# Optimization experiments

Hardware: AMD Instinct MI355X
Metric: run time of the kernel (lower is better)

Reference implementation:

```python
import jax, jax.numpy as jnp
from jax import lax
import numpy as np

# ---- config (repo globals, scaled to a 112x112 feature map of a 448 image) ----
IMG, FEAT = 448, 112
PSTRIDE = IMG // FEAT  # 4 pixels per feature cell
RATIOS = [(16, 16), (12, 20), (20, 12),
          (24, 24), (20, 28), (28, 20),
          (32, 32), (24, 40), (40, 24), (28, 40), (40, 28), (28, 36), (36, 28)]
GROUPS = [(0, 3), (3, 6), (6, 13)]   # ratio groups per NMS scale
N_LIST = [2, 3, 2]
IOU_THRESHS = [0.25, 0.25, 0.25]
BATCH = 256
WINDOW_NUMS = [(FEAT - rh + 1) * (FEAT - rw + 1) for rh, rw in RATIOS]
TOTAL = sum(WINDOW_NUMS)             # 96981
PROPOSALN = sum(N_LIST)              # 7


def _coordinates():
    # Mirrors ComputeCoordinate: box = [x0,y0,x1,y1] in pixels, lefttop clipped to 0.
    parts = []
    for rh, rw in RATIOS:
        nr, nc = FEAT - rh + 1, FEAT - rw + 1
        xi = np.repeat(np.arange(nr), nc).astype(np.float32)
        yi = np.tile(np.arange(nc), nr).astype(np.float32)
        x0 = xi * PSTRIDE - 1.0
        y0 = yi * PSTRIDE - 1.0
        x1 = x0 + rh * PSTRIDE
        y1 = y0 + rw * PSTRIDE
        x0 = np.maximum(x0, 0.0)
        y0 = np.maximum(y0, 0.0)
        parts.append(np.stack([x0, y0, x1, y1], 1))
    return np.concatenate(parts, 0).astype(np.float32)  # (TOTAL, 4)


def setup_inputs() -> dict:
    key = jax.random.key(0)
    x = jax.random.normal(key, (BATCH, 1, FEAT, FEAT), jnp.float32)
    coords = jnp.asarray(_coordinates())
    return {"x": x, "coords": coords, "proposalN": PROPOSALN}


def _nms(scores, coords, n_pick, thresh):
    # Greedy NMS: repeatedly take best-scoring alive window, suppress IoU > thresh.
    # If everything is suppressed before n_pick picks, repeat the last pick (repo behavior).
    areas = (coords[:, 2] - coords[:, 0] + 1.0) * (coords[:, 3] - coords[:, 1] + 1.0)

    def step(state, _):
        alive, last = state
        any_alive = jnp.any(alive)
        idx = jnp.where(any_alive,
                        jnp.argmax(jnp.where(alive, scores, -jnp.inf)).astype(jnp.int32),
                        last)
        box = coords[idx]
        lt = jnp.maximum(coords[:, :2], box[:2])
        rb = jnp.minimum(coords[:, 2:], box[2:])
        w = rb[:, 0] - lt[:, 0] + 1.0
        h = rb[:, 1] - lt[:, 1] + 1.0
        inter = jnp.where((w < 0) | (h < 0), 0.0, w * h)
        iou = inter / (areas + areas[idx] - inter)
        keep = (alive & (iou <= thresh)).at[idx].set(False)
        return (jnp.where(any_alive, keep, alive), idx), idx

    init = (jnp.ones(scores.shape[0], bool), jnp.int32(0))
    return lax.scan(step, init, None, length=n_pick)[1]  # (n_pick,) int32


def _forward(x, coords):
    B = x.shape[0]
    # multiscale sliding-window average scores (AvgPool2d, stride 1, VALID)
    avgs = [lax.reduce_window(x, 0.0, lax.add, (1, 1, rh, rw), (1, 1, 1, 1), 'VALID')
            .reshape(B, -1) / float(rh * rw) for rh, rw in RATIOS]
    all_scores = jnp.concatenate(avgs, 1)  # (B, TOTAL)

    idx_parts = []
    for j, (g0, g1) in enumerate(GROUPS):
        s0 = int(sum(WINDOW_NUMS[:g0]))
        s1 = int(sum(WINDOW_NUMS[:g1]))
        cd = coords[s0:s1]
        nms_j = lambda s, cd=cd, j=j: _nms(s, cd, N_LIST[j], IOU_THRESHS[j])
        picks = jax.vmap(nms_j)(all_scores[:, s0:s1])  # (B, N_LIST[j])
        idx_parts.append(picks + s0)
    proposalN_indices = jnp.concatenate(idx_parts, 1)  # (B, PROPOSALN)
    proposalN_windows_scores = jnp.take_along_axis(all_scores, proposalN_indices, 1)
    window_scores = all_scores  # reshape(batch, -1) of all_scores
    return proposalN_indices, proposalN_windows_scores, window_scores


def reference(x, coords, proposalN):
    assert proposalN == PROPOSALN
    return _forward(x, coords)
```

## Files before the change

kernel.cpp:

```cpp
#include <hip/hip_runtime.h>
#include <math.h>
#include <limits.h>

namespace {
constexpr int kFeat = 112;
constexpr int kBatch = 256;
constexpr int kTotal = 96981;
constexpr int kStride = 115;
constexpr int kNT = 1024;
constexpr int kRH[13] = {16,12,20,24,20,28,32,24,40,28,40,28,36};
constexpr int kRW[13] = {16,20,12,24,28,20,32,40,24,40,28,36,28};
constexpr int kOff[13] = {0,9409,18802,28195,36116,44021,51926,58487,64984,71481,77686,83891,90436};
}

struct NmsShared {
  float rs[kNT / 64];
  int   ri[kNT / 64];
  float shS; int shI;
  float pX0[3], pY0[3], pX1[3], pY1[3], pA[3];
  int   pI[3];
};

__device__ inline void block_argmax(float s, int i, NmsShared* ns) {
  __syncthreads();
#pragma unroll
  for (int off = 32; off > 0; off >>= 1) {
    const float s2 = __shfl_down(s, off, 64);
    const int   i2 = __shfl_down(i, off, 64);
    if (s2 > s || (s2 == s && i2 < i)) { s = s2; i = i2; }
  }
  const int wave = threadIdx.x >> 6;
  if ((threadIdx.x & 63) == 0) { ns->rs[wave] = s; ns->ri[wave] = i; }
  __syncthreads();
  if (threadIdx.x == 0) {
    float bs = ns->rs[0]; int bi = ns->ri[0];
#pragma unroll
    for (int w = 1; w < kNT / 64; ++w) {
      if (ns->rs[w] > bs || (ns->rs[w] == bs && ns->ri[w] < bi)) { bs = ns->rs[w]; bi = ns->ri[w]; }
    }
    ns->shS = bs; ns->shI = bi;
  }
  __syncthreads();
}

template<int RB, int RE>
__device__ inline void pick_store(NmsShared* ns, int k, int slot,
                                  float* __restrict__ out_idx, float* __restrict__ out_sc, int b) {
  if (threadIdx.x == 0) {
    const int pi = ns->shI;
#pragma unroll
    for (int rr = RB; rr < RE; ++rr) {
      const int nr = kFeat - kRH[rr] + 1, nc = kFeat - kRW[rr] + 1;
      if (pi >= kOff[rr] && pi < kOff[rr] + nr * nc) {
        const int l = pi - kOff[rr];
        const int xi = l / nc, yi = l - xi * nc;
        const float x0u = xi * 4.0f - 1.0f, y0u = yi * 4.0f - 1.0f;
        const float x1 = x0u + kRH[rr] * 4.0f, y1 = y0u + kRW[rr] * 4.0f;
        const float x0 = fmaxf(x0u, 0.0f), y0 = fmaxf(y0u, 0.0f);
        ns->pX0[k] = x0; ns->pY0[k] = y0; ns->pX1[k] = x1; ns->pY1[k] = y1;
        ns->pA[k] = (x1 - x0 + 1.0f) * (y1 - y0 + 1.0f);
        ns->pI[k] = pi;
      }
    }
    out_idx[b * 7 + slot + k] = (float)pi;
    out_sc [b * 7 + slot + k] = ns->shS;
  }
  __syncthreads();
}

template<int RB, int RE, int NP, int SLOT>
__device__ inline void nms_group(const float* __restrict__ sat, NmsShared* ns,
                                 float best0, int bi0,
                                 float* __restrict__ out_idx, float* __restrict__ out_sc, int b) {
  const int tid = threadIdx.x;
  block_argmax(best0, bi0, ns);
  pick_store<RB, RE>(ns, 0, SLOT, out_idx, out_sc, b);
  for (int k = 1; k < NP; ++k) {
    float best = -INFINITY; int bi = INT_MAX;
#pragma unroll
    for (int rr = RB; rr < RE; ++rr) {
      const int rh = kRH[rr], rw = kRW[rr];
      const int nr = kFeat - rh + 1, nc = kFeat - rw + 1;
      const float inv = 1.0f / (float)(rh * rw);
      for (int i = tid; i < nr * nc; i += kNT) {
        const int xi = i / nc, yi = i - xi * nc;
        const int gi = kOff[rr] + i;
        const float x0u = xi * 4.0f - 1.0f, y0u = yi * 4.0f - 1.0f;
        const float x1 = x0u + rh * 4.0f, y1 = y0u + rw * 4.0f;
        const float x0 = fmaxf(x0u, 0.0f), y0 = fmaxf(y0u, 0.0f);
        const float a = (x1 - x0 + 1.0f) * (y1 - y0 + 1.0f);
        bool alive = true;
        for (int p = 0; p < k; ++p) {
          if (gi == ns->pI[p]) { alive = false; break; }
          const float lx = fmaxf(x0, ns->pX0[p]), ly = fmaxf(y0, ns->pY0[p]);
          const float rx = fminf(x1, ns->pX1[p]), ry = fminf(y1, ns->pY1[p]);
          const float w = rx - lx + 1.0f, h = ry - ly + 1.0f;
          const float inter = (w < 0.0f || h < 0.0f) ? 0.0f : w * h;
          const float iou = inter / (a + ns->pA[p] - inter);
          if (iou > 0.25f) { alive = false; break; }
        }
        if (alive) {
          const float s = (sat[(xi + rh) * kStride + (yi + rw)]
                         - sat[ xi       * kStride + (yi + rw)]
                         - sat[(xi + rh) * kStride +  yi      ]
                         + sat[ xi       * kStride +  yi      ]) * inv;
          if (s > best) { best = s; bi = gi; }
        }
      }
    }
    block_argmax(best, bi, ns);
    pick_store<RB, RE>(ns, k, SLOT, out_idx, out_sc, b);
  }
}

__global__ __launch_bounds__(kNT, 4) void appm_fused(const float* __restrict__ x,
                                                     float* __restrict__ win,
                                                     float* __restrict__ out_idx,
                                                     float* __restrict__ out_sc) {
  __shared__ float sat[113 * kStride];
  __shared__ NmsShared ns;
  const int b = blockIdx.x;
  const int tid = threadIdx.x;
  const float* xb = x + (size_t)b * kFeat * kFeat;

  for (int j = tid; j < 113; j += kNT) { sat[j] = 0.f; sat[j * kStride] = 0.f; }
  for (int i = tid; i < kFeat * kFeat; i += kNT) {
    const int r = i / kFeat, c = i - r * kFeat;
    sat[(r + 1) * kStride + (c + 1)] = xb[i];
  }
  __syncthreads();

  if (tid < kFeat) {
    float s = 0.f;
    const int row = (tid + 1) * kStride;
    for (int c = 1; c <= kFeat; ++c) { s += sat[row + c]; sat[row + c] = s; }
  }
  __syncthreads();

  if (tid < kFeat) {
    float s = 0.f;
    const int col = tid + 1;
    for (int r = 1; r <= kFeat; ++r) { s += sat[r * kStride + col]; sat[r * kStride + col] = s; }
  }
  __syncthreads();

  float gb[3] = {-INFINITY, -INFINITY, -INFINITY};
  int gbi[3] = {INT_MAX, INT_MAX, INT_MAX};
  float* wb = win + (size_t)b * kTotal;
#pragma unroll
  for (int rr = 0; rr < 13; ++rr) {
    const int g = (rr < 3) ? 0 : (rr < 6) ? 1 : 2;
    const int rh = kRH[rr], rw = kRW[rr];
    const int nr = kFeat - rh + 1, nc = kFeat - rw + 1;
    const float inv = 1.0f / (float)(rh * rw);
    for (int i = tid; i < nr * nc; i += kNT) {
      const int xi = i / nc, yi = i - xi * nc;
      const float s = (sat[(xi + rh) * kStride + (yi + rw)]
                     - sat[ xi       * kStride + (yi + rw)]
                     - sat[(xi + rh) * kStride +  yi      ]
                     + sat[ xi       * kStride +  yi      ]) * inv;
      wb[kOff[rr] + i] = s;
      if (s > gb[g]) { gb[g] = s; gbi[g] = kOff[rr] + i; }
    }
  }

  nms_group<0, 3, 2, 0>(sat, &ns, gb[0], gbi[0], out_idx, out_sc, b);
  nms_group<3, 6, 3, 2>(sat, &ns, gb[1], gbi[1], out_idx, out_sc, b);
  nms_group<6, 13, 2, 5>(sat, &ns, gb[2], gbi[2], out_idx, out_sc, b);
}

extern "C" void kernel_launch(void* const* d_in, const int* in_sizes, int n_in,
                              void* d_out, int out_size, void* d_ws, size_t ws_size,
                              hipStream_t stream) {
  const float* x = (const float*)d_in[0];
  float* out     = (float*)d_out;
  float* out_idx = out;
  float* out_sc  = out + kBatch * 7;
  float* win     = out + 2 * kBatch * 7;

  appm_fused<<<kBatch, kNT, 0, stream>>>(x, win, out_idx, out_sc);
}
```

Baseline: 184.1 us.

## Split each image's NMS groups across three blocks with vectorized SAT window scoring

Launches three blocks per image, one per NMS ratio group. Each block rebuilds the summed-area table and scores only its own windows, so the group work runs in parallel. The SAT build uses float4 loads and a wave-level shuffle scan for the row prefix sums. Window scoring and the suppression passes read four adjacent windows per thread with float4 shared loads (stride padded to 116 for alignment), and the picked boxes are cached in registers. Block size drops to 512 threads with a higher occupancy bound. The cost is building the SAT three times per image, and the groups are unevenly sized (group 2 has seven ratios), so the blocks are imbalanced.

```diff
diff --git a/kernel.cpp b/kernel.cpp
--- a/kernel.cpp
+++ b/kernel.cpp
@@ -6,8 +6,8 @@
 constexpr int kFeat = 112;
 constexpr int kBatch = 256;
 constexpr int kTotal = 96981;
-constexpr int kStride = 115;
-constexpr int kNT = 1024;
+constexpr int kStride = 116;
+constexpr int kNT = 512;
 constexpr int kRH[13] = {16,12,20,24,20,28,32,24,40,28,40,28,36};
 constexpr int kRW[13] = {16,20,12,24,28,20,32,40,24,40,28,36,28};
 constexpr int kOff[13] = {0,9409,18802,28195,36116,44021,51926,58487,64984,71481,77686,83891,90436};
@@ -21,7 +21,7 @@
   int   pI[3];
 };
 
-__device__ inline void block_argmax(float s, int i, NmsShared* ns) {
+__device__ __forceinline__ void block_argmax(float s, int i, NmsShared* ns) {
   __syncthreads();
 #pragma unroll
   for (int off = 32; off > 0; off >>= 1) {
@@ -35,17 +35,53 @@
   if (threadIdx.x == 0) {
     float bs = ns->rs[0]; int bi = ns->ri[0];
 #pragma unroll
-    for (int w = 1; w < kNT / 64; ++w) {
+    for (int w = 1; w < kNT / 64; ++w)
       if (ns->rs[w] > bs || (ns->rs[w] == bs && ns->ri[w] < bi)) { bs = ns->rs[w]; bi = ns->ri[w]; }
-    }
     ns->shS = bs; ns->shI = bi;
   }
   __syncthreads();
 }
 
+__device__ void build_sat(const float* __restrict__ xb, float* __restrict__ sat) {
+  const int tid = threadIdx.x;
+  for (int j = tid; j < kStride; j += kNT) sat[j] = 0.f;
+  for (int r = tid; r < 113; r += kNT) sat[r * kStride] = 0.f;
+  const float4* x4 = (const float4*)xb;
+  for (int i = tid; i < (kFeat * kFeat) / 4; i += kNT) {
+    const float4 v = x4[i];
+    const int r = i / (kFeat / 4);
+    const int c = (i - r * (kFeat / 4)) * 4;
+    float* dst = sat + (r + 1) * kStride + c + 1;
+    dst[0] = v.x; dst[1] = v.y; dst[2] = v.z; dst[3] = v.w;
+  }
+  __syncthreads();
+  const int wave = tid >> 6, lane = tid & 63;
+  for (int r = 1 + wave; r <= kFeat; r += kNT / 64) {
+    float* row = sat + r * kStride;
+    float v = row[1 + lane];
+#pragma unroll
+    for (int d = 1; d < 64; d <<= 1) { const float u = __shfl_up(v, d, 64); if (lane >= d) v += u; }
+    row[1 + lane] = v;
+    const float tot = __shfl(v, 63, 64);
+    const int c = 65 + lane;
+    float w = (c <= kFeat) ? row[c] : 0.f;
+#pragma unroll
+    for (int d = 1; d < 64; d <<= 1) { const float u = __shfl_up(w, d, 64); if (lane >= d) w += u; }
+    if (c <= kFeat) row[c] = w + tot;
+  }
+  __syncthreads();
+  if (tid < kFeat) {
+    const int col = tid + 1;
+    float s = 0.f;
+    for (int r = 1; r <= kFeat; ++r) { s += sat[r * kStride + col]; sat[r * kStride + col] = s; }
+  }
+  __syncthreads();
+}
+
 template<int RB, int RE>
-__device__ inline void pick_store(NmsShared* ns, int k, int slot,
-                                  float* __restrict__ out_idx, float* __restrict__ out_sc, int b) {
+__device__ __forceinline__ void pick_store(NmsShared* ns, int k, int slot,
+                                           float* __restrict__ out_idx,
+                                           float* __restrict__ out_sc, int b) {
   if (threadIdx.x == 0) {
     const int pi = ns->shI;
 #pragma unroll
@@ -69,42 +105,98 @@
 }
 
 template<int RB, int RE, int NP, int SLOT>
-__device__ inline void nms_group(const float* __restrict__ sat, NmsShared* ns,
-                                 float best0, int bi0,
-                                 float* __restrict__ out_idx, float* __restrict__ out_sc, int b) {
+__device__ void run_group(const float* __restrict__ sat, NmsShared* ns,
+                          float* __restrict__ wb,
+                          float* __restrict__ out_idx, float* __restrict__ out_sc, int b) {
   const int tid = threadIdx.x;
-  block_argmax(best0, bi0, ns);
+  float best = -INFINITY; int bi = INT_MAX;
+
+#pragma unroll
+  for (int rr = RB; rr < RE; ++rr) {
+    const int rh = kRH[rr], rw = kRW[rr];
+    const int nr = kFeat - rh + 1, nc = kFeat - rw + 1;
+    const int nqy = (nc + 3) >> 2;
+    const float inv = 1.0f / (float)(rh * rw);
+    for (int q = tid; q < nr * nqy; q += kNT) {
+      const int xi = q / nqy, qy = q - xi * nqy;
+      const int yi0 = qy << 2;
+      const float* u = sat + xi * kStride;
+      const float* d = u + rh * kStride;
+      const float4 U0 = *(const float4*)(u + yi0);
+      const float4 U1 = *(const float4*)(u + yi0 + rw);
+      const float4 D0 = *(const float4*)(d + yi0);
+      const float4 D1 = *(const float4*)(d + yi0 + rw);
+      const float s0 = (D1.x - U1.x - D0.x + U0.x) * inv;
+      const float s1 = (D1.y - U1.y - D0.y + U0.y) * inv;
+      const float s2 = (D1.z - U1.z - D0.z + U0.z) * inv;
+      const float s3 = (D1.w - U1.w - D0.w + U0.w) * inv;
+      const int gi0 = kOff[rr] + xi * nc + yi0;
+      float* w = wb + gi0;
+      const int rem = nc - yi0;
+      w[0] = s0; if (s0 > best) { best = s0; bi = gi0; }
+      if (rem > 1) { w[1] = s1; if (s1 > best) { best = s1; bi = gi0 + 1; } }
+      if (rem > 2) { w[2] = s2; if (s2 > best) { best = s2; bi = gi0 + 2; } }
+      if (rem > 3) { w[3] = s3; if (s3 > best) { best = s3; bi = gi0 + 3; } }
+    }
+  }
+
+  block_argmax(best, bi, ns);
   pick_store<RB, RE>(ns, 0, SLOT, out_idx, out_sc, b);
+
   for (int k = 1; k < NP; ++k) {
-    float best = -INFINITY; int bi = INT_MAX;
+    float px0[NP], py0[NP], px1[NP], py1[NP], pa[NP]; int pix[NP];
+#pragma unroll
+    for (int p = 0; p < NP; ++p) {
+      if (p < k) { px0[p] = ns->pX0[p]; py0[p] = ns->pY0[p]; px1[p] = ns->pX1[p];
+                   py1[p] = ns->pY1[p]; pa[p] = ns->pA[p]; pix[p] = ns->pI[p]; }
+    }
+    best = -INFINITY; bi = INT_MAX;
 #pragma unroll
     for (int rr = RB; rr < RE; ++rr) {
       const int rh = kRH[rr], rw = kRW[rr];
       const int nr = kFeat - rh + 1, nc = kFeat - rw + 1;
+      const int nqy = (nc + 3) >> 2;
       const float inv = 1.0f / (float)(rh * rw);
-      for (int i = tid; i < nr * nc; i += kNT) {
-        const int xi = i / nc, yi = i - xi * nc;
-        const int gi = kOff[rr] + i;
-        const float x0u = xi * 4.0f - 1.0f, y0u = yi * 4.0f - 1.0f;
-        const float x1 = x0u + rh * 4.0f, y1 = y0u + rw * 4.0f;
-        const float x0 = fmaxf(x0u, 0.0f), y0 = fmaxf(y0u, 0.0f);
-        const float a = (x1 - x0 + 1.0f) * (y1 - y0 + 1.0f);
-        bool alive = true;
-        for (int p = 0; p < k; ++p) {
-          if (gi == ns->pI[p]) { alive = false; break; }
-          const float lx = fmaxf(x0, ns->pX0[p]), ly = fmaxf(y0, ns->pY0[p]);
-          const float rx = fminf(x1, ns->pX1[p]), ry = fminf(y1, ns->pY1[p]);
-          const float w = rx - lx + 1.0f, h = ry - ly + 1.0f;
-          const float inter = (w < 0.0f || h < 0.0f) ? 0.0f : w * h;
-          const float iou = inter / (a + ns->pA[p] - inter);
-          if (iou > 0.25f) { alive = false; break; }
-        }
-        if (alive) {
-          const float s = (sat[(xi + rh) * kStride + (yi + rw)]
-                         - sat[ xi       * kStride + (yi + rw)]
-                         - sat[(xi + rh) * kStride +  yi      ]
-                         + sat[ xi       * kStride +  yi      ]) * inv;
-          if (s > best) { best = s; bi = gi; }
+      for (int q = tid; q < nr * nqy; q += kNT) {
+        const int xi = q / nqy, qy = q - xi * nqy;
+        const int yi0 = qy << 2;
+        const float* u = sat + xi * kStride;
+        const float* d = u + rh * kStride;
+        const float4 U0 = *(const float4*)(u + yi0);
+        const float4 U1 = *(const float4*)(u + yi0 + rw);
+        const float4 D0 = *(const float4*)(d + yi0);
+        const float4 D1 = *(const float4*)(d + yi0 + rw);
+        float s4[4];
+        s4[0] = (D1.x - U1.x - D0.x + U0.x) * inv;
+        s4[1] = (D1.y - U1.y - D0.y + U0.y) * inv;
+        s4[2] = (D1.z - U1.z - D0.z + U0.z) * inv;
+        s4[3] = (D1.w - U1.w - D0.w + U0.w) * inv;
+        const float X0u = xi * 4.0f - 1.0f;
+        const float X1 = X0u + rh * 4.0f;
+        const float X0 = fmaxf(X0u, 0.0f);
+        const int gi0 = kOff[rr] + xi * nc + yi0;
+        const int rem = nc - yi0;
+#pragma unroll
+        for (int j = 0; j < 4; ++j) {
+          if (j >= rem) break;
+          const int gi = gi0 + j;
+          const float Y0u = (yi0 + j) * 4.0f - 1.0f;
+          const float Y1 = Y0u + rw * 4.0f;
+          const float Y0 = fmaxf(Y0u, 0.0f);
+          const float A = (X1 - X0 + 1.0f) * (Y1 - Y0 + 1.0f);
+          bool alive = true;
+#pragma unroll
+          for (int p = 0; p < NP; ++p) {
+            if (p >= k) break;
+            if (gi == pix[p]) { alive = false; break; }
+            const float lx = fmaxf(X0, px0[p]), ly = fmaxf(Y0, py0[p]);
+            const float rx = fminf(X1, px1[p]), ry = fminf(Y1, py1[p]);
+            const float w = rx - lx + 1.0f, h = ry - ly + 1.0f;
+            const float inter = (w < 0.0f || h < 0.0f) ? 0.0f : w * h;
+            const float iou = inter / (A + pa[p] - inter);
+            if (iou > 0.25f) { alive = false; break; }
+          }
+          if (alive && s4[j] > best) { best = s4[j]; bi = gi; }
         }
       }
     }
@@ -113,60 +205,21 @@
   }
 }
 
-__global__ __launch_bounds__(kNT, 4) void appm_fused(const float* __restrict__ x,
+__global__ __launch_bounds__(kNT, 6) void appm_fused(const float* __restrict__ x,
                                                      float* __restrict__ win,
                                                      float* __restrict__ out_idx,
                                                      float* __restrict__ out_sc) {
-  __shared__ float sat[113 * kStride];
+  __shared__ __align__(16) float sat[113 * kStride];
   __shared__ NmsShared ns;
-  const int b = blockIdx.x;
-  const int tid = threadIdx.x;
-  const float* xb = x + (size_t)b * kFeat * kFeat;
-
-  for (int j = tid; j < 113; j += kNT) { sat[j] = 0.f; sat[j * kStride] = 0.f; }
-  for (int i = tid; i < kFeat * kFeat; i += kNT) {
-    const int r = i / kFeat, c = i - r * kFeat;
-    sat[(r + 1) * kStride + (c + 1)] = xb[i];
-  }
-  __syncthreads();
-
-  if (tid < kFeat) {
-    float s = 0.f;
-    const int row = (tid + 1) * kStride;
-    for (int c = 1; c <= kFeat; ++c) { s += sat[row + c]; sat[row + c] = s; }
-  }
-  __syncthreads();
-
-  if (tid < kFeat) {
-    float s = 0.f;
-    const int col = tid + 1;
-    for (int r = 1; r <= kFeat; ++r) { s += sat[r * kStride + col]; sat[r * kStride + col] = s; }
-  }
-  __syncthreads();
-
-  float gb[3] = {-INFINITY, -INFINITY, -INFINITY};
-  int gbi[3] = {INT_MAX, INT_MAX, INT_MAX};
+  const int b = blockIdx.x / 3;
+  const int t = blockIdx.x % 3;
+
+  build_sat(x + (size_t)b * kFeat * kFeat, sat);
+
   float* wb = win + (size_t)b * kTotal;
-#pragma unroll
-  for (int rr = 0; rr < 13; ++rr) {
-    const int g = (rr < 3) ? 0 : (rr < 6) ? 1 : 2;
-    const int rh = kRH[rr], rw = kRW[rr];
-    const int nr = kFeat - rh + 1, nc = kFeat - rw + 1;
-    const float inv = 1.0f / (float)(rh * rw);
-    for (int i = tid; i < nr * nc; i += kNT) {
-      const int xi = i / nc, yi = i - xi * nc;
-      const float s = (sat[(xi + rh) * kStride + (yi + rw)]
-                     - sat[ xi       * kStride + (yi + rw)]
-                     - sat[(xi + rh) * kStride +  yi      ]
-                     + sat[ xi       * kStride +  yi      ]) * inv;
-      wb[kOff[rr] + i] = s;
-      if (s > gb[g]) { gb[g] = s; gbi[g] = kOff[rr] + i; }
-    }
-  }
-
-  nms_group<0, 3, 2, 0>(sat, &ns, gb[0], gbi[0], out_idx, out_sc, b);
-  nms_group<3, 6, 3, 2>(sat, &ns, gb[1], gbi[1], out_idx, out_sc, b);
-  nms_group<6, 13, 2, 5>(sat, &ns, gb[2], gbi[2], out_idx, out_sc, b);
+  if (t == 0)       run_group<0, 3, 2, 0>(sat, &ns, wb, out_idx, out_sc, b);
+  else if (t == 1)  run_group<3, 6, 3, 2>(sat, &ns, wb, out_idx, out_sc, b);
+  else              run_group<6, 13, 2, 5>(sat, &ns, wb, out_idx, out_sc, b);
 }
 
 extern "C" void kernel_launch(void* const* d_in, const int* in_sizes, int n_in,
@@ -178,5 +231,5 @@
   float* out_sc  = out + kBatch * 7;
   float* win     = out + 2 * kBatch * 7;
 
-  appm_fused<<<kBatch, kNT, 0, stream>>>(x, win, out_idx, out_sc);
-}
+  appm_fused<<<kBatch * 3, kNT, 0, stream>>>(x, win, out_idx, out_sc);
+}
```

Measured after the change: 180.8 us. About the same (-1.8%).
